# Performance work log

Hardware: AMD Instinct MI355X
Metric: run time of the kernel (lower is better)

## Reference

```python
import jax, jax.numpy as jnp
import numpy as np

ATTRACTION_W = 1.0
REPULSION_W = 1.0
BETA_POS_W = 1.0
BETA_NEG_W = 0.5
K_INST = 256  # max number of distinct instance ids (slice ids)


def setup_inputs() -> dict:
    key = jax.random.key(0)
    B, N, D, K = 4, 65536, 256, K_INST
    k1, k2, k3 = jax.random.split(key, 3)
    beta = jax.random.normal(k1, (B, N, 1), jnp.float32)
    embed = jax.random.normal(k2, (B, N, D), jnp.float32)
    sid = jax.random.randint(k3, (B, N), -1, K)  # -1 = background
    # force exactly one condensation point per instance: hit i (<K) -> sid=i, is_cp
    sid = sid.at[:, :K].set(jnp.broadcast_to(jnp.arange(K), (B, K)))
    is_cp = jnp.zeros((B, N), bool).at[:, :K].set(True)
    return {"beta": beta, "embed": embed, "slice_id": sid, "is_cp": is_cp}


def _loss_single(beta, emb, sid, cp):
    # beta: (N,) logits, emb: (N,D), sid: (N,) int, cp: (N,) bool
    N = sid.shape[0]
    valid = sid >= 0
    cpv = cp & valid  # condensation points with a valid instance id
    # BCE-with-logits: target 1 -> softplus(-x), target 0 -> softplus(x)
    pos = jnp.sum(jnp.where(cpv, jax.nn.softplus(-beta), 0.0)) / jnp.maximum(cpv.sum(), 1)
    noncp = ~cp
    neg = jnp.sum(jnp.where(noncp, jax.nn.softplus(beta), 0.0)) / jnp.maximum(noncp.sum(), 1)
    beta_loss = BETA_POS_W * pos + BETA_NEG_W * neg

    # first CP hit index per instance (segment-min over CP hits), N = "no CP"
    sid_c = jnp.where(valid, sid, 0)
    idx = jnp.arange(N)
    first_cp = jnp.full((K_INST,), N, jnp.int32).at[sid_c].min(
        jnp.where(cpv, idx, N).astype(jnp.int32))
    has_cp = first_cp < N
    cp_emb = emb[jnp.minimum(first_cp, N - 1)]  # (K, D), garbage where no CP

    # attraction: sum over instances of mean ||emb - inst_cp||^2
    d2 = jnp.sum((emb - cp_emb[sid_c]) ** 2, axis=-1)  # (N,)
    w = valid & has_cp[sid_c]
    seg_sum = jnp.zeros((K_INST,), jnp.float32).at[sid_c].add(jnp.where(w, d2, 0.0))
    seg_cnt = jnp.zeros((K_INST,), jnp.float32).at[sid_c].add(w.astype(jnp.float32))
    attraction = jnp.sum(jnp.where(seg_cnt > 0, seg_sum / jnp.maximum(seg_cnt, 1.0), 0.0))
    attraction = attraction * ATTRACTION_W

    # repulsion: mean exp(-||cp_i - cp_j||^2) over all CP pairs (incl. diagonal)
    pd2 = jnp.sum((cp_emb[:, None, :] - cp_emb[None, :, :]) ** 2, axis=-1)  # (K,K)
    pmask = has_cp[:, None] & has_cp[None, :]
    M = has_cp.sum()
    rep = jnp.sum(jnp.where(pmask, jnp.exp(-pd2), 0.0)) / jnp.maximum(M * M, 1)
    rep = jnp.where(M > 1, rep * REPULSION_W, 0.0)

    loss = beta_loss + attraction + rep
    ok = (valid.sum() > 0) & (cpv.sum() > 0)
    return jnp.where(ok, loss, 0.0), ok


def reference(beta, embed, slice_id, is_cp):
    losses, oks = jax.vmap(_loss_single)(beta.squeeze(-1), embed, slice_id, is_cp)
    cnt = oks.sum()
    return jnp.where(cnt > 0, losses.sum() / jnp.maximum(cnt, 1), 0.0)
```

## Files before the change

kernel.cpp:

```cpp
#include <hip/hip_runtime.h>
#include <math.h>

#define K_INST 256
#define ATTRACTION_W 1.0f
#define REPULSION_W 1.0f
#define BETA_POS_W 1.0f
#define BETA_NEG_W 0.5f

typedef float f32x4 __attribute__((ext_vector_type(4)));
typedef int i32x4 __attribute__((ext_vector_type(4)));

__device__ inline float softplusf(float x) {
    return fmaxf(x, 0.f) + log1pf(expf(-fabsf(x)));
}

__device__ inline float waveReduceSumF(float v) {
    for (int o = 32; o; o >>= 1) v += __shfl_xor(v, o);
    return v;
}
__device__ inline int waveReduceSumI(int v) {
    for (int o = 32; o; o >>= 1) v += __shfl_xor(v, o);
    return v;
}

__global__ void stats_kernel(const float* __restrict__ beta,
                             const int* __restrict__ sid,
                             const int* __restrict__ is_cp,
                             int* first_cp,
                             float* pos_sum, float* neg_sum,
                             int* seg_cnt,
                             int* cpv_cnt, int* noncp_cnt, int* valid_cnt,
                             int N) {
    int b = blockIdx.y;
    int base = (blockIdx.x * blockDim.x + threadIdx.x) * 4;
    const float* betaB = beta + (size_t)b * N;
    const int* sidB = sid + (size_t)b * N;
    const int* cpB = is_cp + (size_t)b * N;

    __shared__ int hist[K_INST];
    for (int k = threadIdx.x; k < K_INST; k += blockDim.x) hist[k] = 0;
    __syncthreads();

    i32x4 s4 = *(const i32x4*)(sidB + base);
    i32x4 c4 = *(const i32x4*)(cpB + base);
    f32x4 x4 = *(const f32x4*)(betaB + base);

    float pos = 0.f, neg = 0.f;
    int c_cpv = 0, c_non = 0, c_val = 0;
    #pragma unroll
    for (int e = 0; e < 4; ++e) {
        int s = s4[e], cp = c4[e];
        float x = x4[e];
        bool valid = s >= 0;
        bool cpv = cp && valid;
        if (valid) atomicAdd(&hist[s], 1);
        if (cpv) {
            pos += softplusf(-x);
            c_cpv++;
            atomicMin(&first_cp[b * K_INST + s], base + e);
        }
        if (!cp) {
            neg += softplusf(x);
            c_non++;
        }
        c_val += valid ? 1 : 0;
    }

    __shared__ float sf[2][4];
    __shared__ int si[3][4];
    pos = waveReduceSumF(pos);
    neg = waveReduceSumF(neg);
    c_cpv = waveReduceSumI(c_cpv);
    c_non = waveReduceSumI(c_non);
    c_val = waveReduceSumI(c_val);
    int wave = threadIdx.x >> 6, lane = threadIdx.x & 63;
    if (lane == 0) {
        sf[0][wave] = pos; sf[1][wave] = neg;
        si[0][wave] = c_cpv; si[1][wave] = c_non; si[2][wave] = c_val;
    }
    __syncthreads();
    if (threadIdx.x == 0) {
        float p = sf[0][0] + sf[0][1] + sf[0][2] + sf[0][3];
        float n = sf[1][0] + sf[1][1] + sf[1][2] + sf[1][3];
        int a = si[0][0] + si[0][1] + si[0][2] + si[0][3];
        int c = si[1][0] + si[1][1] + si[1][2] + si[1][3];
        int v = si[2][0] + si[2][1] + si[2][2] + si[2][3];
        if (p != 0.f) atomicAdd(&pos_sum[b], p);
        if (n != 0.f) atomicAdd(&neg_sum[b], n);
        if (a) atomicAdd(&cpv_cnt[b], a);
        if (c) atomicAdd(&noncp_cnt[b], c);
        if (v) atomicAdd(&valid_cnt[b], v);
    }
    for (int k = threadIdx.x; k < K_INST; k += blockDim.x) {
        int h = hist[k];
        if (h) atomicAdd(&seg_cnt[b * K_INST + k], h);
    }
}

__global__ void gather_kernel(const float* __restrict__ embed,
                              const int* __restrict__ first_cp,
                              float* __restrict__ cp_emb,
                              float* __restrict__ cp_embT, int N) {
    int b = blockIdx.y;
    int k = blockIdx.x;
    int src = first_cp[b * K_INST + k];
    if (src >= N) src = N - 1;
    int lane = threadIdx.x;
    const float* embB = embed + (size_t)b * N * 256;
    f32x4 v = ((const f32x4*)(embB + (size_t)src * 256))[lane];
    ((f32x4*)(cp_emb + ((size_t)b * K_INST + k) * 256))[lane] = v;
    float* T = cp_embT + (size_t)b * K_INST * 256;
    int d = lane * 4;
    T[(size_t)(d + 0) * 256 + k] = v[0];
    T[(size_t)(d + 1) * 256 + k] = v[1];
    T[(size_t)(d + 2) * 256 + k] = v[2];
    T[(size_t)(d + 3) * 256 + k] = v[3];
}

__device__ inline float sel8f(const float* v, int lane) {
    float a0 = (lane & 1) ? v[1] : v[0];
    float a1 = (lane & 1) ? v[3] : v[2];
    float a2 = (lane & 1) ? v[5] : v[4];
    float a3 = (lane & 1) ? v[7] : v[6];
    float b0 = (lane & 2) ? a1 : a0;
    float b1 = (lane & 2) ? a3 : a2;
    return (lane & 4) ? b1 : b0;
}
__device__ inline int sel8i(const int* v, int lane) {
    int a0 = (lane & 1) ? v[1] : v[0];
    int a1 = (lane & 1) ? v[3] : v[2];
    int a2 = (lane & 1) ? v[5] : v[4];
    int a3 = (lane & 1) ? v[7] : v[6];
    int b0 = (lane & 2) ? a1 : a0;
    int b1 = (lane & 2) ? a3 : a2;
    return (lane & 4) ? b1 : b0;
}

__global__ void attraction_repulsion_kernel(
        const float* __restrict__ embed,
        const int* __restrict__ sid,
        const int* __restrict__ first_cp,
        const float* __restrict__ cp_emb,
        const float* __restrict__ cp_embT,
        float* seg_sum, float* rep_sum,
        int N, int atr_blocks) {
    int b = blockIdx.y;
    __shared__ __align__(16) char smem[8448];
    __shared__ float sf[4];

    const float* cpB = cp_emb + (size_t)b * K_INST * 256;
    const int* fcB = first_cp + b * K_INST;

    if (blockIdx.x < 32) {
        float (*srow)[264] = (float(*)[264])smem;
        int i0 = blockIdx.x * 8;
        const float* T = cp_embT + (size_t)b * K_INST * 256;
        {
            int r = threadIdx.x >> 5, cc = (threadIdx.x & 31) * 8;
            f32x4 a = *(const f32x4*)(cpB + (size_t)(i0 + r) * 256 + cc);
            f32x4 bv = *(const f32x4*)(cpB + (size_t)(i0 + r) * 256 + cc + 4);
            srow[r][cc + 0] = a[0]; srow[r][cc + 1] = a[1];
            srow[r][cc + 2] = a[2]; srow[r][cc + 3] = a[3];
            srow[r][cc + 4] = bv[0]; srow[r][cc + 5] = bv[1];
            srow[r][cc + 6] = bv[2]; srow[r][cc + 7] = bv[3];
        }
        __syncthreads();

        int j = threadIdx.x;
        bool has_j = fcB[j] < N;
        float acc[8] = {0.f, 0.f, 0.f, 0.f, 0.f, 0.f, 0.f, 0.f};
        for (int d = 0; d < 256; d += 2) {
            float v0 = T[(size_t)d * 256 + j];
            float v1 = T[(size_t)(d + 1) * 256 + j];
            #pragma unroll
            for (int r = 0; r < 8; ++r) {
                float f0 = srow[r][d] - v0;
                float f1 = srow[r][d + 1] - v1;
                acc[r] += f0 * f0 + f1 * f1;
            }
        }
        float val = 0.f;
        #pragma unroll
        for (int r = 0; r < 8; ++r) {
            bool has_i = fcB[i0 + r] < N;
            if (has_i && has_j) val += expf(-acc[r]);
        }
        val = waveReduceSumF(val);
        int wave = threadIdx.x >> 6, lane = threadIdx.x & 63;
        if (lane == 0) sf[wave] = val;
        __syncthreads();
        if (threadIdx.x == 0)
            atomicAdd(&rep_sum[b], sf[0] + sf[1] + sf[2] + sf[3]);
    } else {
        float* s_sum = (float*)smem;
        for (int k = threadIdx.x; k < K_INST; k += blockDim.x) s_sum[k] = 0.f;
        __syncthreads();

        int bx = blockIdx.x - 32;
        int lane = threadIdx.x & 63;
        int wid = bx * 4 + (threadIdx.x >> 6);
        int stride = atr_blocks * 4 * 8;

        const float* embB = embed + (size_t)b * N * 256;
        const int* sidB = sid + (size_t)b * N;

        int i = wid * 8;
        i32x4 sa = {0, 0, 0, 0}, sb = {0, 0, 0, 0};
        if (i < N) {
            sa = __builtin_nontemporal_load((const i32x4*)(sidB + i));
            sb = __builtin_nontemporal_load((const i32x4*)(sidB + i + 4));
        }
        while (i < N) {
            int ss[8] = {sa[0], sa[1], sa[2], sa[3], sb[0], sb[1], sb[2], sb[3]};

            f32x4 e[8];
            #pragma unroll
            for (int j = 0; j < 8; ++j)
                e[j] = __builtin_nontemporal_load(
                    (const f32x4*)(embB + (size_t)(i + j) * 256 + lane * 4));
            f32x4 c[8];
            #pragma unroll
            for (int j = 0; j < 8; ++j) {
                int sc = ss[j] < 0 ? 0 : ss[j];
                c[j] = *(const f32x4*)(cpB + (size_t)sc * 256 + lane * 4);
            }
            int inext = i + stride;
            i32x4 na = {0, 0, 0, 0}, nb = {0, 0, 0, 0};
            if (inext < N) {
                na = __builtin_nontemporal_load((const i32x4*)(sidB + inext));
                nb = __builtin_nontemporal_load((const i32x4*)(sidB + inext + 4));
            }

            float v[8];
            #pragma unroll
            for (int j = 0; j < 8; ++j) {
                float d0 = e[j][0] - c[j][0], d1 = e[j][1] - c[j][1];
                float d2 = e[j][2] - c[j][2], d3 = e[j][3] - c[j][3];
                v[j] = d0 * d0 + d1 * d1 + d2 * d2 + d3 * d3;
            }
            #pragma unroll
            for (int o = 1; o <= 4; o <<= 1) {
                #pragma unroll
                for (int j = 0; j < 8; ++j) v[j] += __shfl_xor(v[j], o);
            }
            float w = sel8f(v, lane & 7);
            #pragma unroll
            for (int o = 8; o <= 32; o <<= 1) w += __shfl_xor(w, o);
            if (lane < 8) {
                int s_sel = sel8i(ss, lane);
                if (s_sel >= 0) atomicAdd(&s_sum[s_sel], w);
            }
            sa = na; sb = nb;
            i = inext;
        }
        __syncthreads();
        for (int k = threadIdx.x; k < K_INST; k += blockDim.x) {
            float v = s_sum[k];
            if (v != 0.f) atomicAdd(&seg_sum[b * K_INST + k], v);
        }
    }
}

__global__ void final_kernel(const int* __restrict__ first_cp,
                             const float* __restrict__ seg_sum,
                             const int* __restrict__ seg_cnt,
                             const float* __restrict__ pos_sum,
                             const float* __restrict__ neg_sum,
                             const float* __restrict__ rep_sum,
                             const int* __restrict__ cpv_cnt,
                             const int* __restrict__ noncp_cnt,
                             const int* __restrict__ valid_cnt,
                             float* out, int N, int B) {
    __shared__ float s_att[4];
    __shared__ int s_m[4];
    float loss_sum = 0.f;
    int ok_cnt = 0;
    int wave = threadIdx.x >> 6, lane = threadIdx.x & 63;
    for (int b = 0; b < B; ++b) {
        int k = threadIdx.x;
        int fc = first_cp[b * K_INST + k];
        int has = (fc < N) ? 1 : 0;
        int cnt = seg_cnt[b * K_INST + k];
        float att = (has && cnt > 0) ? (seg_sum[b * K_INST + k] / (float)cnt) : 0.f;
        att = waveReduceSumF(att);
        has = waveReduceSumI(has);
        if (lane == 0) { s_att[wave] = att; s_m[wave] = has; }
        __syncthreads();
        if (threadIdx.x == 0) {
            float attraction = (s_att[0] + s_att[1] + s_att[2] + s_att[3]) * ATTRACTION_W;
            int M = s_m[0] + s_m[1] + s_m[2] + s_m[3];
            float pos = pos_sum[b] / fmaxf((float)cpv_cnt[b], 1.f);
            float neg = neg_sum[b] / fmaxf((float)noncp_cnt[b], 1.f);
            float beta_loss = BETA_POS_W * pos + BETA_NEG_W * neg;
            float rep = 0.f;
            if (M > 1) {
                float mm = (float)M * (float)M;
                rep = (rep_sum[b] / fmaxf(mm, 1.f)) * REPULSION_W;
            }
            float loss = beta_loss + attraction + rep;
            bool ok = (valid_cnt[b] > 0) && (cpv_cnt[b] > 0);
            if (ok) { loss_sum += loss; ok_cnt += 1; }
        }
        __syncthreads();
    }
    if (threadIdx.x == 0) {
        out[0] = (ok_cnt > 0) ? (loss_sum / (float)ok_cnt) : 0.f;
    }
}

extern "C" void kernel_launch(void* const* d_in, const int* in_sizes, int n_in,
                              void* d_out, int out_size, void* d_ws, size_t ws_size,
                              hipStream_t stream) {
    const float* beta  = (const float*)d_in[0];
    const float* embed = (const float*)d_in[1];
    const int* sid     = (const int*)d_in[2];
    const int* is_cp   = (const int*)d_in[3];
    float* out = (float*)d_out;

    const int N = 65536;
    const int B = in_sizes[0] / N;
    (void)n_in; (void)out_size; (void)ws_size;

    char* ws = (char*)d_ws;
    int*   first_cp  = (int*)(ws + 0);
    float* seg_sum   = (float*)(ws + 4096);
    int*   seg_cnt   = (int*)(ws + 8192);
    float* pos_sum   = (float*)(ws + 12288);
    float* neg_sum   = (float*)(ws + 12352);
    float* rep_sum   = (float*)(ws + 12416);
    int*   cpv_cnt   = (int*)(ws + 12480);
    int*   noncp_cnt = (int*)(ws + 12544);
    int*   valid_cnt = (int*)(ws + 12608);
    float* cp_emb    = (float*)(ws + 16384);
    float* cp_embT   = (float*)(ws + 16384 + (size_t)B * K_INST * 256 * 4);

    hipMemsetAsync(first_cp, 0x7F, (size_t)B * K_INST * 4, stream);
    hipMemsetAsync(ws + 4096, 0, 12288, stream);

    stats_kernel<<<dim3(N / 1024, B), dim3(256), 0, stream>>>(
        beta, sid, is_cp, first_cp, pos_sum, neg_sum, seg_cnt,
        cpv_cnt, noncp_cnt, valid_cnt, N);

    gather_kernel<<<dim3(K_INST, B), dim3(64), 0, stream>>>(
        embed, first_cp, cp_emb, cp_embT, N);

    const int atr_blocks = 480;
    attraction_repulsion_kernel<<<dim3(32 + atr_blocks, B), dim3(256), 0, stream>>>(
        embed, sid, first_cp, cp_emb, cp_embT,
        seg_sum, rep_sum, N, atr_blocks);

    final_kernel<<<dim3(1), dim3(256), 0, stream>>>(
        first_cp, seg_sum, seg_cnt, pos_sum, neg_sum, rep_sum,
        cpv_cnt, noncp_cnt, valid_cnt, out, N, B);
}
```

Baseline: 100.9 us.

## Encode first-CP as reversed max to merge memsets; fuse repulsion into attraction blocks

Stores the first condensation-point index as N-i with atomicMax, so a single zero memset initializes the whole workspace instead of two memsets. The stats kernel now handles one element per thread with four times as many blocks. The attraction and repulsion paths are merged so all 512 blocks stream embeddings, and the first 32 blocks also compute repulsion afterward. This is meant to remove a memset launch and balance work across blocks, at the cost of scalar loads in stats and extra tail work on 32 blocks.

```diff
diff --git a/kernel.cpp b/kernel.cpp
--- a/kernel.cpp
+++ b/kernel.cpp
@@ -26,44 +26,36 @@
 __global__ void stats_kernel(const float* __restrict__ beta,
                              const int* __restrict__ sid,
                              const int* __restrict__ is_cp,
-                             int* first_cp,
+                             int* fc_rev,
                              float* pos_sum, float* neg_sum,
                              int* seg_cnt,
                              int* cpv_cnt, int* noncp_cnt, int* valid_cnt,
                              int N) {
     int b = blockIdx.y;
-    int base = (blockIdx.x * blockDim.x + threadIdx.x) * 4;
-    const float* betaB = beta + (size_t)b * N;
-    const int* sidB = sid + (size_t)b * N;
-    const int* cpB = is_cp + (size_t)b * N;
+    int i = blockIdx.x * blockDim.x + threadIdx.x;
+    size_t gi = (size_t)b * N + i;
 
     __shared__ int hist[K_INST];
     for (int k = threadIdx.x; k < K_INST; k += blockDim.x) hist[k] = 0;
     __syncthreads();
 
-    i32x4 s4 = *(const i32x4*)(sidB + base);
-    i32x4 c4 = *(const i32x4*)(cpB + base);
-    f32x4 x4 = *(const f32x4*)(betaB + base);
-
+    int s = sid[gi];
+    int cp = is_cp[gi];
+    float x = beta[gi];
+
+    bool valid = s >= 0;
+    bool cpv = cp && valid;
     float pos = 0.f, neg = 0.f;
-    int c_cpv = 0, c_non = 0, c_val = 0;
-    #pragma unroll
-    for (int e = 0; e < 4; ++e) {
-        int s = s4[e], cp = c4[e];
-        float x = x4[e];
-        bool valid = s >= 0;
-        bool cpv = cp && valid;
-        if (valid) atomicAdd(&hist[s], 1);
-        if (cpv) {
-            pos += softplusf(-x);
-            c_cpv++;
-            atomicMin(&first_cp[b * K_INST + s], base + e);
-        }
-        if (!cp) {
-            neg += softplusf(x);
-            c_non++;
-        }
-        c_val += valid ? 1 : 0;
+    int c_cpv = 0, c_non = 0, c_val = valid ? 1 : 0;
+    if (valid) atomicAdd(&hist[s], 1);
+    if (cpv) {
+        pos = softplusf(-x);
+        c_cpv = 1;
+        atomicMax(&fc_rev[b * K_INST + s], N - i);
+    }
+    if (!cp) {
+        neg = softplusf(x);
+        c_non = 1;
     }
 
     __shared__ float sf[2][4];
@@ -98,12 +90,12 @@
 }
 
 __global__ void gather_kernel(const float* __restrict__ embed,
-                              const int* __restrict__ first_cp,
+                              const int* __restrict__ fc_rev,
                               float* __restrict__ cp_emb,
                               float* __restrict__ cp_embT, int N) {
     int b = blockIdx.y;
     int k = blockIdx.x;
-    int src = first_cp[b * K_INST + k];
+    int src = N - fc_rev[b * K_INST + k];
     if (src >= N) src = N - 1;
     int lane = threadIdx.x;
     const float* embB = embed + (size_t)b * N * 256;
@@ -139,20 +131,82 @@
 __global__ void attraction_repulsion_kernel(
         const float* __restrict__ embed,
         const int* __restrict__ sid,
-        const int* __restrict__ first_cp,
+        const int* __restrict__ fc_rev,
         const float* __restrict__ cp_emb,
         const float* __restrict__ cp_embT,
-        float* seg_sum, float* rep_sum,
-        int N, int atr_blocks) {
+        float* seg_sum, float* rep_sum, int N) {
     int b = blockIdx.y;
-    __shared__ __align__(16) char smem[8448];
+    __shared__ float s_sum[K_INST];
+    __shared__ float srow[8][264];
     __shared__ float sf[4];
 
     const float* cpB = cp_emb + (size_t)b * K_INST * 256;
-    const int* fcB = first_cp + b * K_INST;
+    int lane = threadIdx.x & 63;
+    int wave = threadIdx.x >> 6;
+
+    for (int k = threadIdx.x; k < K_INST; k += blockDim.x) s_sum[k] = 0.f;
+    __syncthreads();
+
+    int wid = blockIdx.x * 4 + wave;
+    const int stride = 512 * 4 * 8;
+
+    const float* embB = embed + (size_t)b * N * 256;
+    const int* sidB = sid + (size_t)b * N;
+
+    int i = wid * 8;
+    i32x4 sa = __builtin_nontemporal_load((const i32x4*)(sidB + i));
+    i32x4 sb = __builtin_nontemporal_load((const i32x4*)(sidB + i + 4));
+    while (i < N) {
+        int ss[8] = {sa[0], sa[1], sa[2], sa[3], sb[0], sb[1], sb[2], sb[3]};
+
+        f32x4 e[8];
+        #pragma unroll
+        for (int j = 0; j < 8; ++j)
+            e[j] = __builtin_nontemporal_load(
+                (const f32x4*)(embB + (size_t)(i + j) * 256 + lane * 4));
+        f32x4 c[8];
+        #pragma unroll
+        for (int j = 0; j < 8; ++j) {
+            int sc = ss[j] < 0 ? 0 : ss[j];
+            c[j] = *(const f32x4*)(cpB + (size_t)sc * 256 + lane * 4);
+        }
+        int inext = i + stride;
+        i32x4 na = {0, 0, 0, 0}, nb = {0, 0, 0, 0};
+        if (inext < N) {
+            na = __builtin_nontemporal_load((const i32x4*)(sidB + inext));
+            nb = __builtin_nontemporal_load((const i32x4*)(sidB + inext + 4));
+        }
+
+        float v[8];
+        #pragma unroll
+        for (int j = 0; j < 8; ++j) {
+            float d0 = e[j][0] - c[j][0], d1 = e[j][1] - c[j][1];
+            float d2 = e[j][2] - c[j][2], d3 = e[j][3] - c[j][3];
+            v[j] = d0 * d0 + d1 * d1 + d2 * d2 + d3 * d3;
+        }
+        #pragma unroll
+        for (int o = 1; o <= 4; o <<= 1) {
+            #pragma unroll
+            for (int j = 0; j < 8; ++j) v[j] += __shfl_xor(v[j], o);
+        }
+        float w = sel8f(v, lane & 7);
+        #pragma unroll
+        for (int o = 8; o <= 32; o <<= 1) w += __shfl_xor(w, o);
+        if (lane < 8) {
+            int s_sel = sel8i(ss, lane);
+            if (s_sel >= 0) atomicAdd(&s_sum[s_sel], w);
+        }
+        sa = na; sb = nb;
+        i = inext;
+    }
+    __syncthreads();
+    for (int k = threadIdx.x; k < K_INST; k += blockDim.x) {
+        float v = s_sum[k];
+        if (v != 0.f) atomicAdd(&seg_sum[b * K_INST + k], v);
+    }
 
     if (blockIdx.x < 32) {
-        float (*srow)[264] = (float(*)[264])smem;
+        const int* fcB = fc_rev + b * K_INST;
         int i0 = blockIdx.x * 8;
         const float* T = cp_embT + (size_t)b * K_INST * 256;
         {
@@ -167,7 +221,7 @@
         __syncthreads();
 
         int j = threadIdx.x;
-        bool has_j = fcB[j] < N;
+        bool has_j = fcB[j] > 0;
         float acc[8] = {0.f, 0.f, 0.f, 0.f, 0.f, 0.f, 0.f, 0.f};
         for (int d = 0; d < 256; d += 2) {
             float v0 = T[(size_t)d * 256 + j];
@@ -182,86 +236,18 @@
         float val = 0.f;
         #pragma unroll
         for (int r = 0; r < 8; ++r) {
-            bool has_i = fcB[i0 + r] < N;
+            bool has_i = fcB[i0 + r] > 0;
             if (has_i && has_j) val += expf(-acc[r]);
         }
         val = waveReduceSumF(val);
-        int wave = threadIdx.x >> 6, lane = threadIdx.x & 63;
         if (lane == 0) sf[wave] = val;
         __syncthreads();
         if (threadIdx.x == 0)
             atomicAdd(&rep_sum[b], sf[0] + sf[1] + sf[2] + sf[3]);
-    } else {
-        float* s_sum = (float*)smem;
-        for (int k = threadIdx.x; k < K_INST; k += blockDim.x) s_sum[k] = 0.f;
-        __syncthreads();
-
-        int bx = blockIdx.x - 32;
-        int lane = threadIdx.x & 63;
-        int wid = bx * 4 + (threadIdx.x >> 6);
-        int stride = atr_blocks * 4 * 8;
-
-        const float* embB = embed + (size_t)b * N * 256;
-        const int* sidB = sid + (size_t)b * N;
-
-        int i = wid * 8;
-        i32x4 sa = {0, 0, 0, 0}, sb = {0, 0, 0, 0};
-        if (i < N) {
-            sa = __builtin_nontemporal_load((const i32x4*)(sidB + i));
-            sb = __builtin_nontemporal_load((const i32x4*)(sidB + i + 4));
-        }
-        while (i < N) {
-            int ss[8] = {sa[0], sa[1], sa[2], sa[3], sb[0], sb[1], sb[2], sb[3]};
-
-            f32x4 e[8];
-            #pragma unroll
-            for (int j = 0; j < 8; ++j)
-                e[j] = __builtin_nontemporal_load(
-                    (const f32x4*)(embB + (size_t)(i + j) * 256 + lane * 4));
-            f32x4 c[8];
-            #pragma unroll
-            for (int j = 0; j < 8; ++j) {
-                int sc = ss[j] < 0 ? 0 : ss[j];
-                c[j] = *(const f32x4*)(cpB + (size_t)sc * 256 + lane * 4);
-            }
-            int inext = i + stride;
-            i32x4 na = {0, 0, 0, 0}, nb = {0, 0, 0, 0};
-            if (inext < N) {
-                na = __builtin_nontemporal_load((const i32x4*)(sidB + inext));
-                nb = __builtin_nontemporal_load((const i32x4*)(sidB + inext + 4));
-            }
-
-            float v[8];
-            #pragma unroll
-            for (int j = 0; j < 8; ++j) {
-                float d0 = e[j][0] - c[j][0], d1 = e[j][1] - c[j][1];
-                float d2 = e[j][2] - c[j][2], d3 = e[j][3] - c[j][3];
-                v[j] = d0 * d0 + d1 * d1 + d2 * d2 + d3 * d3;
-            }
-            #pragma unroll
-            for (int o = 1; o <= 4; o <<= 1) {
-                #pragma unroll
-                for (int j = 0; j < 8; ++j) v[j] += __shfl_xor(v[j], o);
-            }
-            float w = sel8f(v, lane & 7);
-            #pragma unroll
-            for (int o = 8; o <= 32; o <<= 1) w += __shfl_xor(w, o);
-            if (lane < 8) {
-                int s_sel = sel8i(ss, lane);
-                if (s_sel >= 0) atomicAdd(&s_sum[s_sel], w);
-            }
-            sa = na; sb = nb;
-            i = inext;
-        }
-        __syncthreads();
-        for (int k = threadIdx.x; k < K_INST; k += blockDim.x) {
-            float v = s_sum[k];
-            if (v != 0.f) atomicAdd(&seg_sum[b * K_INST + k], v);
-        }
-    }
-}
-
-__global__ void final_kernel(const int* __restrict__ first_cp,
+    }
+}
+
+__global__ void final_kernel(const int* __restrict__ fc_rev,
                              const float* __restrict__ seg_sum,
                              const int* __restrict__ seg_cnt,
                              const float* __restrict__ pos_sum,
@@ -278,8 +264,7 @@
     int wave = threadIdx.x >> 6, lane = threadIdx.x & 63;
     for (int b = 0; b < B; ++b) {
         int k = threadIdx.x;
-        int fc = first_cp[b * K_INST + k];
-        int has = (fc < N) ? 1 : 0;
+        int has = (fc_rev[b * K_INST + k] > 0) ? 1 : 0;
         int cnt = seg_cnt[b * K_INST + k];
         float att = (has && cnt > 0) ? (seg_sum[b * K_INST + k] / (float)cnt) : 0.f;
         att = waveReduceSumF(att);
@@ -322,7 +307,7 @@
     (void)n_in; (void)out_size; (void)ws_size;
 
     char* ws = (char*)d_ws;
-    int*   first_cp  = (int*)(ws + 0);
+    int*   fc_rev    = (int*)(ws + 0);
     float* seg_sum   = (float*)(ws + 4096);
     int*   seg_cnt   = (int*)(ws + 8192);
     float* pos_sum   = (float*)(ws + 12288);
@@ -334,22 +319,19 @@
     float* cp_emb    = (float*)(ws + 16384);
     float* cp_embT   = (float*)(ws + 16384 + (size_t)B * K_INST * 256 * 4);
 
-    hipMemsetAsync(first_cp, 0x7F, (size_t)B * K_INST * 4, stream);
-    hipMemsetAsync(ws + 4096, 0, 12288, stream);
-
-    stats_kernel<<<dim3(N / 1024, B), dim3(256), 0, stream>>>(
-        beta, sid, is_cp, first_cp, pos_sum, neg_sum, seg_cnt,
+    hipMemsetAsync(ws, 0, 16384, stream);
+
+    stats_kernel<<<dim3(N / 256, B), dim3(256), 0, stream>>>(
+        beta, sid, is_cp, fc_rev, pos_sum, neg_sum, seg_cnt,
         cpv_cnt, noncp_cnt, valid_cnt, N);
 
     gather_kernel<<<dim3(K_INST, B), dim3(64), 0, stream>>>(
-        embed, first_cp, cp_emb, cp_embT, N);
-
-    const int atr_blocks = 480;
-    attraction_repulsion_kernel<<<dim3(32 + atr_blocks, B), dim3(256), 0, stream>>>(
-        embed, sid, first_cp, cp_emb, cp_embT,
-        seg_sum, rep_sum, N, atr_blocks);
+        embed, fc_rev, cp_emb, cp_embT, N);
+
+    attraction_repulsion_kernel<<<dim3(512, B), dim3(256), 0, stream>>>(
+        embed, sid, fc_rev, cp_emb, cp_embT, seg_sum, rep_sum, N);
 
     final_kernel<<<dim3(1), dim3(256), 0, stream>>>(
-        first_cp, seg_sum, seg_cnt, pos_sum, neg_sum, rep_sum,
+        fc_rev, seg_sum, seg_cnt, pos_sum, neg_sum, rep_sum,
         cpv_cnt, noncp_cnt, valid_cnt, out, N, B);
 }
```

Result: slower. 124.0 us (+22.9%).

## Sort hits by instance via counting scatter before attraction pass

Applied to the files above, without the earlier changes.

Adds a scatter kernel that builds a per-batch ordering of hit indices grouped by instance id, using a prefix scan of segment counts and global cursors. The attraction pass reads this order and gathers embedding rows indirectly, so segment atomics and centroid reads are grouped by instance. First-CP tracking switches to atomicMax on a reversed index so the workspace can be zero-initialised in one memset. This adds an extra kernel and a memset over an order buffer, and it turns sequential embedding streaming into row-granular gathers.

```diff
diff --git a/kernel.cpp b/kernel.cpp
--- a/kernel.cpp
+++ b/kernel.cpp
@@ -26,7 +26,7 @@
 __global__ void stats_kernel(const float* __restrict__ beta,
                              const int* __restrict__ sid,
                              const int* __restrict__ is_cp,
-                             int* first_cp,
+                             int* fc_rev,
                              float* pos_sum, float* neg_sum,
                              int* seg_cnt,
                              int* cpv_cnt, int* noncp_cnt, int* valid_cnt,
@@ -57,7 +57,7 @@
         if (cpv) {
             pos += softplusf(-x);
             c_cpv++;
-            atomicMin(&first_cp[b * K_INST + s], base + e);
+            atomicMax(&fc_rev[b * K_INST + s], N - (base + e));
         }
         if (!cp) {
             neg += softplusf(x);
@@ -97,13 +97,76 @@
     }
 }
 
+__global__ void scatter_kernel(const int* __restrict__ sid,
+                               const int* __restrict__ seg_cnt,
+                               int* cursor, int* order, int N) {
+    int b = blockIdx.y;
+    int base = (blockIdx.x * blockDim.x + threadIdx.x) * 4;
+    const int* sidB = sid + (size_t)b * N;
+    int* orderB = order + (size_t)b * N;
+
+    __shared__ int lhist[K_INST];
+    __shared__ int lcnt[K_INST];
+    __shared__ int lbase[K_INST];
+    __shared__ int scanA[K_INST];
+    __shared__ int scanB[K_INST];
+
+    int t = threadIdx.x;
+    lhist[t] = 0; lcnt[t] = 0;
+    __syncthreads();
+
+    i32x4 s4 = *(const i32x4*)(sidB + base);
+    #pragma unroll
+    for (int e = 0; e < 4; ++e) {
+        if (s4[e] >= 0) atomicAdd(&lhist[s4[e]], 1);
+    }
+    __syncthreads();
+
+    int myCnt = seg_cnt[b * K_INST + t];
+    scanA[t] = myCnt;
+    __syncthreads();
+    int* src = scanA; int* dst = scanB;
+    #pragma unroll
+    for (int off = 1; off < K_INST; off <<= 1) {
+        int v = src[t] + ((t >= off) ? src[t - off] : 0);
+        dst[t] = v;
+        __syncthreads();
+        int* tmp = src; src = dst; dst = tmp;
+    }
+    int segStart = src[t] - myCnt;
+    int h = lhist[t];
+    lbase[t] = (h > 0) ? atomicAdd(&cursor[b * K_INST + t], h) : 0;
+    __syncthreads();
+
+    #pragma unroll
+    for (int e = 0; e < 4; ++e) {
+        int s = s4[e];
+        if (s >= 0) {
+            int r = atomicAdd(&lcnt[s], 1);
+        }
+    }
+    scanA[t] = segStart;
+    __syncthreads();
+    lcnt[t] = 0;
+    __syncthreads();
+    #pragma unroll
+    for (int e = 0; e < 4; ++e) {
+        int s = s4[e];
+        if (s >= 0) {
+            int r = atomicAdd(&lcnt[s], 1);
+            int slot = scanA[s] + lbase[s] + r;
+            orderB[slot] = ((base + e) << 8) | s;
+        }
+    }
+}
+
 __global__ void gather_kernel(const float* __restrict__ embed,
-                              const int* __restrict__ first_cp,
+                              const int* __restrict__ fc_rev,
                               float* __restrict__ cp_emb,
                               float* __restrict__ cp_embT, int N) {
     int b = blockIdx.y;
     int k = blockIdx.x;
-    int src = first_cp[b * K_INST + k];
+    int src = N - fc_rev[b * K_INST + k];
     if (src >= N) src = N - 1;
     int lane = threadIdx.x;
     const float* embB = embed + (size_t)b * N * 256;
@@ -138,8 +201,8 @@
 
 __global__ void attraction_repulsion_kernel(
         const float* __restrict__ embed,
-        const int* __restrict__ sid,
-        const int* __restrict__ first_cp,
+        const int* __restrict__ order,
+        const int* __restrict__ fc_rev,
         const float* __restrict__ cp_emb,
         const float* __restrict__ cp_embT,
         float* seg_sum, float* rep_sum,
@@ -149,10 +212,10 @@
     __shared__ float sf[4];
 
     const float* cpB = cp_emb + (size_t)b * K_INST * 256;
-    const int* fcB = first_cp + b * K_INST;
 
     if (blockIdx.x < 32) {
         float (*srow)[264] = (float(*)[264])smem;
+        const int* fcB = fc_rev + b * K_INST;
         int i0 = blockIdx.x * 8;
         const float* T = cp_embT + (size_t)b * K_INST * 256;
         {
@@ -167,7 +230,7 @@
         __syncthreads();
 
         int j = threadIdx.x;
-        bool has_j = fcB[j] < N;
+        bool has_j = fcB[j] > 0;
         float acc[8] = {0.f, 0.f, 0.f, 0.f, 0.f, 0.f, 0.f, 0.f};
         for (int d = 0; d < 256; d += 2) {
             float v0 = T[(size_t)d * 256 + j];
@@ -182,7 +245,7 @@
         float val = 0.f;
         #pragma unroll
         for (int r = 0; r < 8; ++r) {
-            bool has_i = fcB[i0 + r] < N;
+            bool has_i = fcB[i0 + r] > 0;
             if (has_i && has_j) val += expf(-acc[r]);
         }
         val = waveReduceSumF(val);
@@ -202,33 +265,37 @@
         int stride = atr_blocks * 4 * 8;
 
         const float* embB = embed + (size_t)b * N * 256;
-        const int* sidB = sid + (size_t)b * N;
+        const int* ordB = order + (size_t)b * N;
 
         int i = wid * 8;
-        i32x4 sa = {0, 0, 0, 0}, sb = {0, 0, 0, 0};
+        i32x4 ea = {-1, -1, -1, -1}, eb = {-1, -1, -1, -1};
         if (i < N) {
-            sa = __builtin_nontemporal_load((const i32x4*)(sidB + i));
-            sb = __builtin_nontemporal_load((const i32x4*)(sidB + i + 4));
+            ea = __builtin_nontemporal_load((const i32x4*)(ordB + i));
+            eb = __builtin_nontemporal_load((const i32x4*)(ordB + i + 4));
         }
         while (i < N) {
-            int ss[8] = {sa[0], sa[1], sa[2], sa[3], sb[0], sb[1], sb[2], sb[3]};
+            int en[8] = {ea[0], ea[1], ea[2], ea[3], eb[0], eb[1], eb[2], eb[3]};
+            int ss[8];
+            #pragma unroll
+            for (int j = 0; j < 8; ++j) ss[j] = en[j] < 0 ? -1 : (en[j] & 255);
 
             f32x4 e[8];
             #pragma unroll
-            for (int j = 0; j < 8; ++j)
-                e[j] = __builtin_nontemporal_load(
-                    (const f32x4*)(embB + (size_t)(i + j) * 256 + lane * 4));
+            for (int j = 0; j < 8; ++j) {
+                int off = ((en[j] < 0 ? 0 : (en[j] >> 8)) << 8) | (lane << 2);
+                e[j] = __builtin_nontemporal_load((const f32x4*)(embB + off));
+            }
             f32x4 c[8];
             #pragma unroll
             for (int j = 0; j < 8; ++j) {
-                int sc = ss[j] < 0 ? 0 : ss[j];
-                c[j] = *(const f32x4*)(cpB + (size_t)sc * 256 + lane * 4);
+                int off = ((ss[j] < 0 ? 0 : ss[j]) << 8) | (lane << 2);
+                c[j] = *(const f32x4*)(cpB + off);
             }
             int inext = i + stride;
-            i32x4 na = {0, 0, 0, 0}, nb = {0, 0, 0, 0};
+            i32x4 na = {-1, -1, -1, -1}, nb = {-1, -1, -1, -1};
             if (inext < N) {
-                na = __builtin_nontemporal_load((const i32x4*)(sidB + inext));
-                nb = __builtin_nontemporal_load((const i32x4*)(sidB + inext + 4));
+                na = __builtin_nontemporal_load((const i32x4*)(ordB + inext));
+                nb = __builtin_nontemporal_load((const i32x4*)(ordB + inext + 4));
             }
 
             float v[8];
@@ -250,7 +317,7 @@
                 int s_sel = sel8i(ss, lane);
                 if (s_sel >= 0) atomicAdd(&s_sum[s_sel], w);
             }
-            sa = na; sb = nb;
+            ea = na; eb = nb;
             i = inext;
         }
         __syncthreads();
@@ -261,7 +328,7 @@
     }
 }
 
-__global__ void final_kernel(const int* __restrict__ first_cp,
+__global__ void final_kernel(const int* __restrict__ fc_rev,
                              const float* __restrict__ seg_sum,
                              const int* __restrict__ seg_cnt,
                              const float* __restrict__ pos_sum,
@@ -278,8 +345,7 @@
     int wave = threadIdx.x >> 6, lane = threadIdx.x & 63;
     for (int b = 0; b < B; ++b) {
         int k = threadIdx.x;
-        int fc = first_cp[b * K_INST + k];
-        int has = (fc < N) ? 1 : 0;
+        int has = (fc_rev[b * K_INST + k] > 0) ? 1 : 0;
         int cnt = seg_cnt[b * K_INST + k];
         float att = (has && cnt > 0) ? (seg_sum[b * K_INST + k] / (float)cnt) : 0.f;
         att = waveReduceSumF(att);
@@ -322,34 +388,39 @@
     (void)n_in; (void)out_size; (void)ws_size;
 
     char* ws = (char*)d_ws;
-    int*   first_cp  = (int*)(ws + 0);
+    int*   fc_rev    = (int*)(ws + 0);
     float* seg_sum   = (float*)(ws + 4096);
     int*   seg_cnt   = (int*)(ws + 8192);
-    float* pos_sum   = (float*)(ws + 12288);
-    float* neg_sum   = (float*)(ws + 12352);
-    float* rep_sum   = (float*)(ws + 12416);
-    int*   cpv_cnt   = (int*)(ws + 12480);
-    int*   noncp_cnt = (int*)(ws + 12544);
-    int*   valid_cnt = (int*)(ws + 12608);
-    float* cp_emb    = (float*)(ws + 16384);
-    float* cp_embT   = (float*)(ws + 16384 + (size_t)B * K_INST * 256 * 4);
-
-    hipMemsetAsync(first_cp, 0x7F, (size_t)B * K_INST * 4, stream);
-    hipMemsetAsync(ws + 4096, 0, 12288, stream);
+    int*   cursor    = (int*)(ws + 12288);
+    float* pos_sum   = (float*)(ws + 16384);
+    float* neg_sum   = (float*)(ws + 16448);
+    float* rep_sum   = (float*)(ws + 16512);
+    int*   cpv_cnt   = (int*)(ws + 16576);
+    int*   noncp_cnt = (int*)(ws + 16640);
+    int*   valid_cnt = (int*)(ws + 16704);
+    int*   order     = (int*)(ws + 20480);
+    float* cp_emb    = (float*)(ws + 20480 + (size_t)B * N * 4);
+    float* cp_embT   = cp_emb + (size_t)B * K_INST * 256;
+
+    hipMemsetAsync(ws, 0, 20480, stream);
+    hipMemsetAsync(order, 0xFF, (size_t)B * N * 4, stream);
 
     stats_kernel<<<dim3(N / 1024, B), dim3(256), 0, stream>>>(
-        beta, sid, is_cp, first_cp, pos_sum, neg_sum, seg_cnt,
+        beta, sid, is_cp, fc_rev, pos_sum, neg_sum, seg_cnt,
         cpv_cnt, noncp_cnt, valid_cnt, N);
 
+    scatter_kernel<<<dim3(N / 1024, B), dim3(256), 0, stream>>>(
+        sid, seg_cnt, cursor, order, N);
+
     gather_kernel<<<dim3(K_INST, B), dim3(64), 0, stream>>>(
-        embed, first_cp, cp_emb, cp_embT, N);
-
-    const int atr_blocks = 480;
+        embed, fc_rev, cp_emb, cp_embT, N);
+
+    const int atr_blocks = 512;
     attraction_repulsion_kernel<<<dim3(32 + atr_blocks, B), dim3(256), 0, stream>>>(
-        embed, sid, first_cp, cp_emb, cp_embT,
+        embed, order, fc_rev, cp_emb, cp_embT,
         seg_sum, rep_sum, N, atr_blocks);
 
     final_kernel<<<dim3(1), dim3(256), 0, stream>>>(
-        first_cp, seg_sum, seg_cnt, pos_sum, neg_sum, rep_sum,
+        fc_rev, seg_sum, seg_cnt, pos_sum, neg_sum, rep_sum,
         cpv_cnt, noncp_cnt, valid_cnt, out, N, B);
 }
```

New measurement: 105.0 us. 1.04x slower.
